# Performance work log

Hardware: AMD Instinct MI355X
Metric: run time of the kernel (lower is better)

The kernel has to match this reference:

```python
import jax, jax.numpy as jnp
import numpy as np

M, K, N = 4096, 4096, 11008

def setup_inputs() -> dict:
    key = jax.random.key(0)
    k1, k2, k3, k4, k5 = jax.random.split(key, 5)
    x = jax.random.normal(k1, (M, K), dtype=jnp.float32)
    # int8 weights stored as int32 carrier (values in [-128, 127])
    weight = jax.random.randint(k2, (N, K), -128, 128, dtype=jnp.int32)
    # per-channel dequant scale, small positive values
    deq_scale = jax.random.uniform(k3, (N,), dtype=jnp.float32, minval=1e-4, maxval=2e-3)
    # static per-tensor activation scale
    input_scale = jax.random.uniform(k4, (1,), dtype=jnp.float32, minval=0.02, maxval=0.05)
    input_offset = jnp.zeros((1,), dtype=jnp.int32)
    quant_bias = jax.random.randint(k5, (N,), -1000, 1000, dtype=jnp.int32)
    return {"x": x, "weight": weight, "deq_scale": deq_scale,
            "input_scale": input_scale, "input_offset": input_offset,
            "quant_bias": quant_bias}

def reference(x, weight, deq_scale, input_scale, input_offset, quant_bias):
    # Static per-tensor activation quantization to int8
    x_q = jnp.clip(jnp.round(x / input_scale) + input_offset.astype(jnp.float32),
                   -128.0, 127.0).astype(jnp.int32)  # [M, K]
    # int8 GEMM accumulated in int32 (weight stored [N, K], i.e. transposed)
    acc = jnp.einsum('mk,nk->mn', x_q, weight)  # [M, N] int32
    # add int32 quant bias, per-channel dequant to fp32
    out = (acc + quant_bias[None, :]).astype(jnp.float32) * deq_scale[None, :]
    return out
```

## Files before the change

### kernel.cpp

```cpp
#include <hip/hip_runtime.h>
#include <cstdint>
#include <cstddef>

#define M_DIM 4096
#define K_DIM 4096
#define N_DIM 11008
#define BK 64
#define NTM 32
#define NTN 86

typedef int   int4v   __attribute__((ext_vector_type(4)));
typedef float float4v __attribute__((ext_vector_type(4)));

__device__ __forceinline__ void gload_lds16(const void* g, void* l) {
  __builtin_amdgcn_global_load_lds(
      (const __attribute__((address_space(1))) unsigned int*)g,
      (__attribute__((address_space(3))) unsigned int*)l, 16, 0, 0);
}

__global__ void quant_x_kernel(const float* __restrict__ x,
                               const float* __restrict__ scale_p,
                               const int* __restrict__ off_p,
                               signed char* __restrict__ xq, int total16) {
  const float inv = 1.0f / scale_p[0];
  const float off = (float)off_p[0];
  int tid = blockIdx.x * blockDim.x + threadIdx.x;
  int stride = gridDim.x * blockDim.x;
  const float4v* x4 = (const float4v*)x;
  int4v* out4 = (int4v*)xq;
  for (int i = tid; i < total16; i += stride) {
    int4v o;
#pragma unroll
    for (int j = 0; j < 4; ++j) {
      float4v v = x4[(size_t)i * 4 + j];
      int r = 0;
#pragma unroll
      for (int e = 0; e < 4; ++e) {
        float q = rintf(v[e] * inv) + off;
        q = fminf(fmaxf(q, -128.0f), 127.0f);
        int qi = (int)q;
        r |= (qi & 0xff) << (8 * e);
      }
      o[j] = r;
    }
    out4[i] = o;
  }
}

__global__ void pack_w_kernel(const int* __restrict__ w,
                              signed char* __restrict__ wq, int total16) {
  int tid = blockIdx.x * blockDim.x + threadIdx.x;
  int stride = gridDim.x * blockDim.x;
  const int4v* w4 = (const int4v*)w;
  int4v* out4 = (int4v*)wq;
  for (int i = tid; i < total16; i += stride) {
    int4v o;
#pragma unroll
    for (int j = 0; j < 4; ++j) {
      int4v v = w4[(size_t)i * 4 + j];
      o[j] = (v[0] & 0xff) | ((v[1] & 0xff) << 8) |
             ((v[2] & 0xff) << 16) | ((v[3] & 0xff) << 24);
    }
    out4[i] = o;
  }
}

__global__ __launch_bounds__(256, 2) void gemm_i8_kernel(
    const signed char* __restrict__ A,
    const signed char* __restrict__ B,
    const int* __restrict__ qbias,
    const float* __restrict__ dscale,
    float* __restrict__ out) {
  __shared__ __attribute__((aligned(16))) signed char lA[128 * BK];
  __shared__ __attribute__((aligned(16))) signed char lB[128 * BK];

  const int t = threadIdx.x;
  const int lane = t & 63;
  const int wv = t >> 6;

  int bid = blockIdx.x;
  const int nwg = NTM * NTN;
  const int cpx = nwg >> 3;
  int swz = (bid & 7) * cpx + (bid >> 3);
  const int GROUPM = 8;
  const int width = GROUPM * NTN;
  int group = swz / width;
  int rem = swz % width;
  int tm = group * GROUPM + (rem % GROUPM);
  int tn = rem / GROUPM;

  const signed char* Ab = A + (size_t)tm * 128 * K_DIM;
  const signed char* Bb = B + (size_t)tn * 128 * K_DIM;

  const int srow = wv * 16 + (lane >> 2);
  const int scol = (lane & 3) * 16;

  int4v acc[4][4];
#pragma unroll
  for (int i = 0; i < 4; ++i)
#pragma unroll
    for (int j = 0; j < 4; ++j) acc[i][j] = (int4v){0, 0, 0, 0};

  const int wm = (wv >> 1) * 64;
  const int wn = (wv & 1) * 64;
  const int fr = lane & 15;
  const int klo = (lane >> 4) * 16;

  for (int kt = 0; kt < K_DIM / BK; ++kt) {
    const signed char* ga = Ab + kt * BK;
    const signed char* gb = Bb + kt * BK;
    gload_lds16(ga + (size_t)srow * K_DIM + scol,        lA + wv * 1024);
    gload_lds16(ga + (size_t)(srow + 64) * K_DIM + scol, lA + 4096 + wv * 1024);
    gload_lds16(gb + (size_t)srow * K_DIM + scol,        lB + wv * 1024);
    gload_lds16(gb + (size_t)(srow + 64) * K_DIM + scol, lB + 4096 + wv * 1024);
    __syncthreads();

    int4v afrag[4], bfrag[4];
#pragma unroll
    for (int mi = 0; mi < 4; ++mi)
      afrag[mi] = *(const int4v*)(lA + (wm + mi * 16 + fr) * BK + klo);
#pragma unroll
    for (int ni = 0; ni < 4; ++ni)
      bfrag[ni] = *(const int4v*)(lB + (wn + ni * 16 + fr) * BK + klo);

#pragma unroll
    for (int mi = 0; mi < 4; ++mi)
#pragma unroll
      for (int ni = 0; ni < 4; ++ni)
        acc[mi][ni] = __builtin_amdgcn_mfma_i32_16x16x64_i8(
            afrag[mi], bfrag[ni], acc[mi][ni], 0, 0, 0);

    __syncthreads();
  }

  const int col = lane & 15;
  const int rb = (lane >> 4) * 4;
  const int gm0 = tm * 128 + wm;
  const int gn0 = tn * 128 + wn;
#pragma unroll
  for (int ni = 0; ni < 4; ++ni) {
    int gn = gn0 + ni * 16 + col;
    float ds = dscale[gn];
    int qb = qbias[gn];
#pragma unroll
    for (int mi = 0; mi < 4; ++mi) {
      int gm = gm0 + mi * 16 + rb;
#pragma unroll
      for (int j = 0; j < 4; ++j) {
        out[(size_t)(gm + j) * N_DIM + gn] = (float)(acc[mi][ni][j] + qb) * ds;
      }
    }
  }
}

extern "C" void kernel_launch(void* const* d_in, const int* in_sizes, int n_in,
                              void* d_out, int out_size, void* d_ws, size_t ws_size,
                              hipStream_t stream) {
  const float* x      = (const float*)d_in[0];
  const int*   w      = (const int*)d_in[1];
  const float* dscale = (const float*)d_in[2];
  const float* iscale = (const float*)d_in[3];
  const int*   ioff   = (const int*)d_in[4];
  const int*   qbias  = (const int*)d_in[5];
  float* out = (float*)d_out;

  const size_t xq_bytes = (size_t)M_DIM * K_DIM;
  const size_t wq_bytes = (size_t)N_DIM * K_DIM;
  if (ws_size < xq_bytes + wq_bytes) return;

  signed char* xq = (signed char*)d_ws;
  signed char* wq = (signed char*)d_ws + xq_bytes;

  quant_x_kernel<<<2048, 256, 0, stream>>>(x, iscale, ioff, xq, M_DIM * K_DIM / 16);
  pack_w_kernel<<<2048, 256, 0, stream>>>(w, wq, N_DIM * K_DIM / 16);
  gemm_i8_kernel<<<NTM * NTN, 256, 0, stream>>>(xq, wq, qbias, dscale, out);
}
```

Measured before the change: 285.3 us.

## Use 256x256 tiles with a 3-stage LDS ring and split-phase MFMA pipeline

The int8 GEMM moves from 128x128 tiles with 4 waves and a single LDS buffer to 256x256 tiles with 8 waves. Global-to-LDS loads now go through a 3-deep ring buffer and are issued two K-steps ahead, interleaved with two half-tile MFMA phases separated by barriers and s_setprio. The LDS layout is changed to fragment-major so each lane reads its MFMA operand as one contiguous 16-byte chunk. The aim is to overlap memory with compute and raise data reuse per tile, at the cost of more registers per wave (32 accumulators) and fewer, larger workgroups.

After: 288.1 us. No clear change (+1.0%).

```diff
diff --git a/kernel.cpp b/kernel.cpp
--- a/kernel.cpp
+++ b/kernel.cpp
@@ -5,9 +5,15 @@
 #define M_DIM 4096
 #define K_DIM 4096
 #define N_DIM 11008
-#define BK 64
-#define NTM 32
-#define NTN 86
+#define BM 256
+#define BN 256
+#define BKI 64
+#define NT (K_DIM / BKI)
+#define NTM (M_DIM / BM)
+#define NTN (N_DIM / BN)
+#define TILE_A_BYTES (BM * BKI)
+#define RING_STRIDE (2 * TILE_A_BYTES)
+#define RING 3
 
 typedef int   int4v   __attribute__((ext_vector_type(4)));
 typedef float float4v __attribute__((ext_vector_type(4)));
@@ -65,90 +71,125 @@
   }
 }
 
-__global__ __launch_bounds__(256, 2) void gemm_i8_kernel(
+__global__ __launch_bounds__(512, 2) void gemm_i8_kernel(
     const signed char* __restrict__ A,
     const signed char* __restrict__ B,
     const int* __restrict__ qbias,
     const float* __restrict__ dscale,
     float* __restrict__ out) {
-  __shared__ __attribute__((aligned(16))) signed char lA[128 * BK];
-  __shared__ __attribute__((aligned(16))) signed char lB[128 * BK];
-
-  const int t = threadIdx.x;
-  const int lane = t & 63;
-  const int wv = t >> 6;
+  __shared__ __attribute__((aligned(16))) signed char lds[RING * RING_STRIDE];
+
+  const int tid  = threadIdx.x;
+  const int lane = tid & 63;
+  const int wv   = tid >> 6;
+  const int wr   = wv >> 2;
+  const int wc   = wv & 3;
 
   int bid = blockIdx.x;
-  const int nwg = NTM * NTN;
-  const int cpx = nwg >> 3;
-  int swz = (bid & 7) * cpx + (bid >> 3);
-  const int GROUPM = 8;
-  const int width = GROUPM * NTN;
-  int group = swz / width;
-  int rem = swz % width;
-  int tm = group * GROUPM + (rem % GROUPM);
-  int tn = rem / GROUPM;
-
-  const signed char* Ab = A + (size_t)tm * 128 * K_DIM;
-  const signed char* Bb = B + (size_t)tn * 128 * K_DIM;
-
-  const int srow = wv * 16 + (lane >> 2);
-  const int scol = (lane & 3) * 16;
-
-  int4v acc[4][4];
-#pragma unroll
-  for (int i = 0; i < 4; ++i)
+  int swz = (bid & 7) * ((NTM * NTN) >> 3) + (bid >> 3);
+  int tm = swz & (NTM - 1);
+  int tn = swz >> 4;
+
+  const signed char* Ab = A + (size_t)tm * BM * K_DIM;
+  const signed char* Bb = B + (size_t)tn * BN * K_DIM;
+
+  const int fA    = wv * 2;
+  const int srow  = fA * 16 + (lane & 15);
+  const int koff  = (lane >> 4) * 16;
+  const signed char* gA0 = Ab + (size_t)srow * K_DIM + koff;
+  const signed char* gA1 = gA0 + (size_t)16 * K_DIM;
+  const signed char* gB0 = Bb + (size_t)srow * K_DIM + koff;
+  const signed char* gB1 = gB0 + (size_t)16 * K_DIM;
+  const int dstA = fA * 1024;
+  const int dstB = TILE_A_BYTES + fA * 1024;
+
+#define STAGE_A(kt, roff) do { \
+    gload_lds16(gA0 + (size_t)(kt) * BKI, lds + (roff) + dstA); \
+    gload_lds16(gA1 + (size_t)(kt) * BKI, lds + (roff) + dstA + 1024); } while (0)
+#define STAGE_B(kt, roff) do { \
+    gload_lds16(gB0 + (size_t)(kt) * BKI, lds + (roff) + dstB); \
+    gload_lds16(gB1 + (size_t)(kt) * BKI, lds + (roff) + dstB + 1024); } while (0)
+
+  const int rdA = (wr * 8) * 1024 + lane * 16;
+  const int rdB = TILE_A_BYTES + (wc * 4) * 1024 + lane * 16;
+
+  int4v acc[8][4];
+#pragma unroll
+  for (int i = 0; i < 8; ++i)
 #pragma unroll
     for (int j = 0; j < 4; ++j) acc[i][j] = (int4v){0, 0, 0, 0};
 
-  const int wm = (wv >> 1) * 64;
-  const int wn = (wv & 1) * 64;
-  const int fr = lane & 15;
-  const int klo = (lane >> 4) * 16;
-
-  for (int kt = 0; kt < K_DIM / BK; ++kt) {
-    const signed char* ga = Ab + kt * BK;
-    const signed char* gb = Bb + kt * BK;
-    gload_lds16(ga + (size_t)srow * K_DIM + scol,        lA + wv * 1024);
-    gload_lds16(ga + (size_t)(srow + 64) * K_DIM + scol, lA + 4096 + wv * 1024);
-    gload_lds16(gb + (size_t)srow * K_DIM + scol,        lB + wv * 1024);
-    gload_lds16(gb + (size_t)(srow + 64) * K_DIM + scol, lB + 4096 + wv * 1024);
-    __syncthreads();
-
-    int4v afrag[4], bfrag[4];
-#pragma unroll
-    for (int mi = 0; mi < 4; ++mi)
-      afrag[mi] = *(const int4v*)(lA + (wm + mi * 16 + fr) * BK + klo);
+  STAGE_A(0, 0);
+  STAGE_B(0, 0);
+  STAGE_A(1, RING_STRIDE);
+  STAGE_B(1, RING_STRIDE);
+  asm volatile("s_waitcnt vmcnt(4)" ::: "memory");
+  __builtin_amdgcn_s_barrier();
+
+  int roff = 0;
+  for (int kt = 0; kt < NT; ++kt) {
+    int nxt = roff + 2 * RING_STRIDE;
+    if (nxt >= RING * RING_STRIDE) nxt -= RING * RING_STRIDE;
+
+    int4v bfr[4], afr[4];
 #pragma unroll
     for (int ni = 0; ni < 4; ++ni)
-      bfrag[ni] = *(const int4v*)(lB + (wn + ni * 16 + fr) * BK + klo);
-
+      bfr[ni] = *(const int4v*)(lds + roff + rdB + ni * 1024);
+#pragma unroll
+    for (int mi = 0; mi < 4; ++mi)
+      afr[mi] = *(const int4v*)(lds + roff + rdA + mi * 1024);
+    if (kt + 2 < NT) STAGE_A(kt + 2, nxt);
+    __builtin_amdgcn_s_barrier();
+    asm volatile("s_waitcnt lgkmcnt(0)" ::: "memory");
+    __builtin_amdgcn_s_setprio(1);
 #pragma unroll
     for (int mi = 0; mi < 4; ++mi)
 #pragma unroll
       for (int ni = 0; ni < 4; ++ni)
         acc[mi][ni] = __builtin_amdgcn_mfma_i32_16x16x64_i8(
-            afrag[mi], bfrag[ni], acc[mi][ni], 0, 0, 0);
-
-    __syncthreads();
-  }
+            afr[mi], bfr[ni], acc[mi][ni], 0, 0, 0);
+    __builtin_amdgcn_s_setprio(0);
+    __builtin_amdgcn_s_barrier();
+
+#pragma unroll
+    for (int mi = 0; mi < 4; ++mi)
+      afr[mi] = *(const int4v*)(lds + roff + rdA + (mi + 4) * 1024);
+    if (kt + 2 < NT) STAGE_B(kt + 2, nxt);
+    __builtin_amdgcn_s_barrier();
+    asm volatile("s_waitcnt lgkmcnt(0)" ::: "memory");
+    __builtin_amdgcn_s_setprio(1);
+#pragma unroll
+    for (int mi = 0; mi < 4; ++mi)
+#pragma unroll
+      for (int ni = 0; ni < 4; ++ni)
+        acc[mi + 4][ni] = __builtin_amdgcn_mfma_i32_16x16x64_i8(
+            afr[mi], bfr[ni], acc[mi + 4][ni], 0, 0, 0);
+    __builtin_amdgcn_s_setprio(0);
+    if (kt + 2 < NT) asm volatile("s_waitcnt vmcnt(4)" ::: "memory");
+    else             asm volatile("s_waitcnt vmcnt(0)" ::: "memory");
+    __builtin_amdgcn_s_barrier();
+
+    roff += RING_STRIDE;
+    if (roff >= RING * RING_STRIDE) roff -= RING * RING_STRIDE;
+  }
+#undef STAGE_A
+#undef STAGE_B
 
   const int col = lane & 15;
-  const int rb = (lane >> 4) * 4;
-  const int gm0 = tm * 128 + wm;
-  const int gn0 = tn * 128 + wn;
+  const int rb  = (lane >> 4) * 4;
+  const int gm0 = tm * BM + wr * 128;
+  const int gn0 = tn * BN + wc * 64;
 #pragma unroll
   for (int ni = 0; ni < 4; ++ni) {
     int gn = gn0 + ni * 16 + col;
     float ds = dscale[gn];
     int qb = qbias[gn];
 #pragma unroll
-    for (int mi = 0; mi < 4; ++mi) {
+    for (int mi = 0; mi < 8; ++mi) {
       int gm = gm0 + mi * 16 + rb;
 #pragma unroll
-      for (int j = 0; j < 4; ++j) {
+      for (int j = 0; j < 4; ++j)
         out[(size_t)(gm + j) * N_DIM + gn] = (float)(acc[mi][ni][j] + qb) * ds;
-      }
     }
   }
 }
@@ -173,5 +214,5 @@
 
   quant_x_kernel<<<2048, 256, 0, stream>>>(x, iscale, ioff, xq, M_DIM * K_DIM / 16);
   pack_w_kernel<<<2048, 256, 0, stream>>>(w, wq, N_DIM * K_DIM / 16);
-  gemm_i8_kernel<<<NTM * NTN, 256, 0, stream>>>(xq, wq, qbias, dscale, out);
-}
+  gemm_i8_kernel<<<NTM * NTN, 512, 0, stream>>>(xq, wq, qbias, dscale, out);
+}
```
